# Kernel optimization log

Hardware: AMD Instinct MI355X
Metric: run time of the kernel (lower is better)

Reference implementation:

```python
import jax, jax.numpy as jnp
import numpy as np


def setup_inputs() -> dict:
    key = jax.random.key(0)
    T, B, I, H = 512, 64, 512, 512
    k = 1.0 / np.sqrt(H)
    ks = jax.random.split(key, 5)
    x = jax.random.normal(ks[0], (T, B, I), dtype=jnp.float32)
    w_ih = jax.random.uniform(ks[1], (H, I), jnp.float32, -k, k)
    w_hh = jax.random.uniform(ks[2], (H, H), jnp.float32, -k, k)
    b_ih = jax.random.uniform(ks[3], (H,), jnp.float32, -k, k)
    b_hh = jax.random.uniform(ks[4], (H,), jnp.float32, -k, k)
    return {"x": x, "w_ih": w_ih, "w_hh": w_hh, "b_ih": b_ih, "b_hh": b_hh}


def reference(x, w_ih, w_hh, b_ih, b_hh):
    # Single-layer Elman RNN, batch_first=False: x is [T, B, I].
    # h_t = tanh(x_t @ W_ih^T + b_ih + h_{t-1} @ W_hh^T + b_hh)
    T, B, _ = x.shape
    H = w_hh.shape[0]
    # Precompute input projections for all timesteps in one big GEMM.
    xproj = jnp.einsum('tbi,hi->tbh', x, w_ih) + b_ih + b_hh  # [T, B, H]

    def step(h, xp_t):
        h_new = jnp.tanh(xp_t + h @ w_hh.T)
        return h_new, h_new

    h0 = jnp.zeros((B, H), dtype=x.dtype)
    h_n, output = jax.lax.scan(step, h0, xproj)
    # torch-style h_n has a leading num_layers dim
    return output, h_n[None]
```

## Files before the change

### kernel.cpp

```cpp
#include <hip/hip_runtime.h>
#include <hip/hip_fp16.h>

#define T_STEPS 512
#define BATCH   64
#define HID     512

#define SCH_REG  40
#define SCH_LDS  10
#define SCH_SA   7
#define SCH_SB   7

#define X16_OFF   0u
#define X16_BYTES (16777216u * 2u)
#define WIH_OFF   (X16_OFF + X16_BYTES)
#define WIH_BYTES (262144u * 2u)
#define WHH_OFF   (WIH_OFF + WIH_BYTES)
#define WHH_BYTES (262144u * 2u)
#define WS_FULL   (WHH_OFF + WHH_BYTES)

typedef _Float16 half2v  __attribute__((ext_vector_type(2)));
typedef short    short8  __attribute__((ext_vector_type(8)));
typedef float    f32x4   __attribute__((ext_vector_type(4)));
union F4H { float4 f; half2v h[4]; };

__device__ inline float dot2f(half2v a, half2v b, float c) {
    return __builtin_amdgcn_fdot2(a, b, c, false);
}
__device__ inline unsigned short f2bf(float f) {
    unsigned u = __builtin_bit_cast(unsigned, f);
    return (unsigned short)((u + 0x7FFFu + ((u >> 16) & 1u)) >> 16);
}

__global__ __launch_bounds__(256) void cvt_f16(const float* __restrict__ w,
                                               __half* __restrict__ o) {
    const int i = (blockIdx.x * 256 + threadIdx.x) * 4;
    float4 v = *(const float4*)(w + i);
    __half2 p0; p0.x = __float2half(v.x); p0.y = __float2half(v.y);
    __half2 p1; p1.x = __float2half(v.z); p1.y = __float2half(v.w);
    *(__half2*)(o + i)     = p0;
    *(__half2*)(o + i + 2) = p1;
}

__global__ __launch_bounds__(256) void cvt_bf16(const float* __restrict__ s,
                                                unsigned short* __restrict__ o) {
    const int i = (blockIdx.x * 256 + threadIdx.x) * 4;
    float4 v = *(const float4*)(s + i);
    ushort4 r = {f2bf(v.x), f2bf(v.y), f2bf(v.z), f2bf(v.w)};
    *(ushort4*)(o + i) = r;
}

__global__ __launch_bounds__(256) void xproj_mfma(
    const unsigned short* __restrict__ x16,
    const unsigned short* __restrict__ w16,
    const float* __restrict__ b_ih, const float* __restrict__ b_hh,
    float* __restrict__ out)
{
    __shared__ __align__(16) unsigned short As[128][40];
    __shared__ __align__(16) unsigned short Bs[128][40];

    const int tid   = threadIdx.x;
    const int mBase = blockIdx.y * 128;
    const int nBase = blockIdx.x * 128;
    const int wave  = tid >> 6, lane = tid & 63;
    const int wy    = wave >> 1, wx = wave & 1;
    const int quad  = lane >> 4, l15 = lane & 15;
    const int lr    = tid >> 2;
    const int lk    = (tid & 3) * 8;

    f32x4 acc[4][4] = {};

    const size_t arow0 = (size_t)(mBase + lr) * 512 + lk;
    const size_t brow0 = (size_t)(nBase + lr) * 512 + lk;

    for (int k0 = 0; k0 < 512; k0 += 32) {
        int4 a0 = *(const int4*)(x16 + arow0 + k0);
        int4 a1 = *(const int4*)(x16 + arow0 + (size_t)64 * 512 + k0);
        int4 b0 = *(const int4*)(w16 + brow0 + k0);
        int4 b1 = *(const int4*)(w16 + brow0 + (size_t)64 * 512 + k0);
        __syncthreads();
        *(int4*)&As[lr][lk]      = a0;
        *(int4*)&As[lr + 64][lk] = a1;
        *(int4*)&Bs[lr][lk]      = b0;
        *(int4*)&Bs[lr + 64][lk] = b1;
        __syncthreads();

        short8 af[4], bf[4];
#pragma unroll
        for (int mt = 0; mt < 4; ++mt)
            af[mt] = *(const short8*)&As[wy * 64 + mt * 16 + l15][quad * 8];
#pragma unroll
        for (int nt = 0; nt < 4; ++nt)
            bf[nt] = *(const short8*)&Bs[wx * 64 + nt * 16 + l15][quad * 8];
#pragma unroll
        for (int mt = 0; mt < 4; ++mt)
#pragma unroll
            for (int nt = 0; nt < 4; ++nt)
                acc[mt][nt] = __builtin_amdgcn_mfma_f32_16x16x32_bf16(
                    af[mt], bf[nt], acc[mt][nt], 0, 0, 0);
    }

    float bias[4]; int coln[4];
#pragma unroll
    for (int nt = 0; nt < 4; ++nt) {
        coln[nt] = nBase + wx * 64 + nt * 16 + l15;
        bias[nt] = b_ih[coln[nt]] + b_hh[coln[nt]];
    }
#pragma unroll
    for (int mt = 0; mt < 4; ++mt)
#pragma unroll
        for (int r = 0; r < 4; ++r) {
            const int row = mBase + wy * 64 + mt * 16 + quad * 4 + r;
#pragma unroll
            for (int nt = 0; nt < 4; ++nt)
                out[(size_t)row * 512 + coln[nt]] = acc[mt][nt][r] + bias[nt];
        }
}

__global__ __launch_bounds__(256) void xproj_gemm(
    const float* __restrict__ x, const float* __restrict__ w_ih,
    const float* __restrict__ b_ih, const float* __restrict__ b_hh,
    float* __restrict__ out)
{
    __shared__ __align__(16) float As[16][68];
    __shared__ __align__(16) float Bs[16][68];

    const int tid   = threadIdx.x;
    const int tx    = tid & 15;
    const int ty    = tid >> 4;
    const int mBase = blockIdx.y * 64;
    const int nBase = blockIdx.x * 64;
    const int ldr   = tid >> 2;
    const int ldk   = (tid & 3) * 4;

    float acc[4][4] = {};
    const float* aptr = x    + (size_t)(mBase + ldr) * 512 + ldk;
    const float* bptr = w_ih + (size_t)(nBase + ldr) * 512 + ldk;

    for (int k0 = 0; k0 < 512; k0 += 16) {
        float4 av = *(const float4*)(aptr + k0);
        float4 bv = *(const float4*)(bptr + k0);
        __syncthreads();
        As[ldk + 0][ldr] = av.x; As[ldk + 1][ldr] = av.y;
        As[ldk + 2][ldr] = av.z; As[ldk + 3][ldr] = av.w;
        Bs[ldk + 0][ldr] = bv.x; Bs[ldk + 1][ldr] = bv.y;
        Bs[ldk + 2][ldr] = bv.z; Bs[ldk + 3][ldr] = bv.w;
        __syncthreads();
#pragma unroll
        for (int kk = 0; kk < 16; ++kk) {
            float4 a = *(const float4*)&As[kk][ty * 4];
            float4 b = *(const float4*)&Bs[kk][tx * 4];
            float ar[4] = {a.x, a.y, a.z, a.w};
            float br[4] = {b.x, b.y, b.z, b.w};
#pragma unroll
            for (int i = 0; i < 4; ++i)
#pragma unroll
                for (int j = 0; j < 4; ++j)
                    acc[i][j] = fmaf(ar[i], br[j], acc[i][j]);
        }
    }
    const int n0 = nBase + tx * 4;
    float bias[4];
#pragma unroll
    for (int j = 0; j < 4; ++j) bias[j] = b_ih[n0 + j] + b_hh[n0 + j];
#pragma unroll
    for (int i = 0; i < 4; ++i) {
        const int m = mBase + ty * 4 + i;
        float4 v = {acc[i][0] + bias[0], acc[i][1] + bias[1],
                    acc[i][2] + bias[2], acc[i][3] + bias[3]};
        *(float4*)(out + (size_t)m * 512 + n0) = v;
    }
}

#define ACC4(WF, G) do {                                        \
    F4H hh_; hh_.f = *(const float4*)(hrow + (G) * 8);          \
    F4H ww_; ww_.f = (WF);                                      \
    a0 = dot2f(ww_.h[0], hh_.h[0], a0);                         \
    a1 = dot2f(ww_.h[1], hh_.h[1], a1);                         \
    a2 = dot2f(ww_.h[2], hh_.h[2], a2);                         \
    a3 = dot2f(ww_.h[3], hh_.h[3], a3); } while (0)

__global__ __launch_bounds__(512)
__attribute__((amdgpu_waves_per_eu(2, 2)))
void rnn_scan4(const __half* __restrict__ w16, float* __restrict__ out)
{
    __shared__ __align__(16) float4 wlds[SCH_LDS][HID];
    __shared__ __align__(16) __half hbuf[2][HID];

    const int b = blockIdx.x;
    const int j = threadIdx.x;

    const __half* wrow = w16 + (size_t)j * HID;

    float4 wreg[SCH_REG];
#pragma unroll
    for (int c = 0; c < SCH_REG; ++c)
        wreg[c] = *(const float4*)(wrow + c * 8);

#pragma unroll
    for (int c = 0; c < SCH_LDS; ++c)
        wlds[c][j] = *(const float4*)(wrow + (SCH_REG + c) * 8);

    hbuf[0][j] = __float2half(0.f);
    __syncthreads();

    float* outb = out + (size_t)b * HID + j;
    const size_t stride = (size_t)BATCH * HID;
    const __half* wstr = wrow + (SCH_REG + SCH_LDS) * 8;

    int cur = 0;
    float hn = 0.f;
    float xp_next = outb[0];

    for (int t = 0; t < T_STEPS; ++t) {
        const float xp = xp_next;
        const int tn = (t + 1 < T_STEPS) ? (t + 1) : t;
        xp_next = outb[(size_t)tn * stride];

        const __half* hrow = hbuf[cur];

        float4 wa[SCH_SA];
#pragma unroll
        for (int c = 0; c < SCH_SA; ++c)
            wa[c] = *(const float4*)(wstr + c * 8);

        float a0 = xp, a1 = 0.f, a2 = 0.f, a3 = 0.f;

#pragma unroll
        for (int c = 0; c < 20; ++c) ACC4(wreg[c], c);

#pragma unroll
        for (int c = 0; c < SCH_SA; ++c)
            ACC4(wa[c], SCH_REG + SCH_LDS + c);

        float4 wb[SCH_SB];
#pragma unroll
        for (int c = 0; c < SCH_SB; ++c)
            wb[c] = *(const float4*)(wstr + (SCH_SA + c) * 8);

#pragma unroll
        for (int c = 20; c < SCH_REG; ++c) ACC4(wreg[c], c);
#pragma unroll
        for (int c = 0; c < SCH_LDS; ++c) {
            float4 wf = wlds[c][j];
            ACC4(wf, SCH_REG + c);
        }

#pragma unroll
        for (int c = 0; c < SCH_SB; ++c)
            ACC4(wb[c], SCH_REG + SCH_LDS + SCH_SA + c);

        float s = (a0 + a1) + (a2 + a3);
        s = fminf(fmaxf(s, -15.f), 15.f);
        const float e = __expf(2.f * s);
        hn = (e - 1.f) * __builtin_amdgcn_rcpf(e + 1.f);

        outb[(size_t)t * stride] = hn;
        hbuf[cur ^ 1][j] = __float2half(hn);
        __syncthreads();
        cur ^= 1;
    }
    out[(size_t)T_STEPS * stride + (size_t)b * HID + j] = hn;
}

__global__ __launch_bounds__(512) void rnn_scan_f32(const float* __restrict__ w,
                                                    float* __restrict__ out)
{
    __shared__ __align__(16) __half hs[2][HID];
    const int b = blockIdx.x;
    const int j = threadIdx.x;

    hs[0][j] = __float2half(0.f);
    __syncthreads();

    const float* wrow32 = w + (size_t)j * HID;
    float* outb = out + (size_t)b * HID + j;
    int cur = 0;
    float hn = 0.f;

    for (int t = 0; t < T_STEPS; ++t) {
        float a0 = outb[(size_t)t * (BATCH * HID)];
        float a1 = 0.f, a2 = 0.f, a3 = 0.f;
#pragma unroll 4
        for (int k0 = 0; k0 < HID; k0 += 8) {
            float4 w0 = *(const float4*)(wrow32 + k0);
            float4 w1 = *(const float4*)(wrow32 + k0 + 4);
            F4H h; h.f = *(const float4*)(&hs[cur][k0]);
            float2 h0 = __half22float2(*(__half2*)&h.h[0]);
            float2 h1 = __half22float2(*(__half2*)&h.h[1]);
            float2 h2 = __half22float2(*(__half2*)&h.h[2]);
            float2 h3 = __half22float2(*(__half2*)&h.h[3]);
            a0 = fmaf(w0.x, h0.x, a0); a1 = fmaf(w0.y, h0.y, a1);
            a2 = fmaf(w0.z, h1.x, a2); a3 = fmaf(w0.w, h1.y, a3);
            a0 = fmaf(w1.x, h2.x, a0); a1 = fmaf(w1.y, h2.y, a1);
            a2 = fmaf(w1.z, h3.x, a2); a3 = fmaf(w1.w, h3.y, a3);
        }
        hn = tanhf((a0 + a1) + (a2 + a3));
        outb[(size_t)t * (BATCH * HID)] = hn;
        hs[cur ^ 1][j] = __float2half(hn);
        __syncthreads();
        cur ^= 1;
    }
    out[(size_t)T_STEPS * BATCH * HID + (size_t)b * HID + j] = hn;
}

extern "C" void kernel_launch(void* const* d_in, const int* in_sizes, int n_in,
                              void* d_out, int out_size, void* d_ws, size_t ws_size,
                              hipStream_t stream) {
    const float* x    = (const float*)d_in[0];
    const float* w_ih = (const float*)d_in[1];
    const float* w_hh = (const float*)d_in[2];
    const float* b_ih = (const float*)d_in[3];
    const float* b_hh = (const float*)d_in[4];
    float* out = (float*)d_out;

    char* ws = (char*)d_ws;
    const bool full = ws_size >= (size_t)WS_FULL;
    const bool mid  = ws_size >= (size_t)WHH_BYTES;

    if (full) {
        unsigned short* x16   = (unsigned short*)(ws + X16_OFF);
        unsigned short* wih16 = (unsigned short*)(ws + WIH_OFF);
        __half*         whh16 = (__half*)(ws + WHH_OFF);
        cvt_bf16<<<16384, 256, 0, stream>>>(x, x16);
        cvt_bf16<<<256,   256, 0, stream>>>(w_ih, wih16);
        cvt_f16 <<<256,   256, 0, stream>>>(w_hh, whh16);
        xproj_mfma<<<dim3(4, 256), 256, 0, stream>>>(x16, wih16, b_ih, b_hh, out);
        rnn_scan4<<<BATCH, HID, 0, stream>>>(whh16, out);
    } else if (mid) {
        __half* whh16 = (__half*)ws;
        cvt_f16<<<256, 256, 0, stream>>>(w_hh, whh16);
        xproj_gemm<<<dim3(8, 512), 256, 0, stream>>>(x, w_ih, b_ih, b_hh, out);
        rnn_scan4<<<BATCH, HID, 0, stream>>>(whh16, out);
    } else {
        xproj_gemm<<<dim3(8, 512), 256, 0, stream>>>(x, w_ih, b_ih, b_hh, out);
        rnn_scan_f32<<<BATCH, HID, 0, stream>>>(w_hh, out);
    }
}
```

Before: 892.1 us.

## Use MFMA recurrent scan over 16-batch groups with fp16 tiled xproj

Replaces the per-batch dot2 recurrent kernel with an MFMA-based scan. Each of 4 blocks handles 16 batch rows and keeps W_hh fragments in registers and LDS, while the hidden state lives in LDS as fp16. The input conversion of x is fused into the xproj GEMM, which now writes fp16 projections in a tiled layout matched to the scan's MFMA output fragments. This removes one full pass over x and cuts the recurrent dot-product work per step. The cost is only 4 active CUs for the serial scan and extra fp16 rounding of the projections and hidden state.

```diff
diff --git a/kernel.cpp b/kernel.cpp
--- a/kernel.cpp
+++ b/kernel.cpp
@@ -4,24 +4,29 @@
 #define T_STEPS 512
 #define BATCH   64
 #define HID     512
+
+#define NB      16
+#define AK_LDS  12
 
 #define SCH_REG  40
 #define SCH_LDS  10
 #define SCH_SA   7
 #define SCH_SB   7
 
-#define X16_OFF   0u
-#define X16_BYTES (16777216u * 2u)
-#define WIH_OFF   (X16_OFF + X16_BYTES)
+#define XP16_OFF  0u
+#define XP16_BYTES (16777216u * 2u)
+#define WIH_OFF   (XP16_OFF + XP16_BYTES)
 #define WIH_BYTES (262144u * 2u)
 #define WHH_OFF   (WIH_OFF + WIH_BYTES)
 #define WHH_BYTES (262144u * 2u)
 #define WS_FULL   (WHH_OFF + WHH_BYTES)
 
 typedef _Float16 half2v  __attribute__((ext_vector_type(2)));
+typedef _Float16 half4v  __attribute__((ext_vector_type(4)));
+typedef _Float16 half8   __attribute__((ext_vector_type(8)));
 typedef short    short8  __attribute__((ext_vector_type(8)));
 typedef float    f32x4   __attribute__((ext_vector_type(4)));
-union F4H { float4 f; half2v h[4]; };
+union F4H  { float4 f; half2v h[4]; };
 
 __device__ inline float dot2f(half2v a, half2v b, float c) {
     return __builtin_amdgcn_fdot2(a, b, c, false);
@@ -50,10 +55,10 @@
 }
 
 __global__ __launch_bounds__(256) void xproj_mfma(
-    const unsigned short* __restrict__ x16,
+    const float* __restrict__ x,
     const unsigned short* __restrict__ w16,
     const float* __restrict__ b_ih, const float* __restrict__ b_hh,
-    float* __restrict__ out)
+    __half* __restrict__ xp16)
 {
     __shared__ __align__(16) unsigned short As[128][40];
     __shared__ __align__(16) unsigned short Bs[128][40];
@@ -73,13 +78,24 @@
     const size_t brow0 = (size_t)(nBase + lr) * 512 + lk;
 
     for (int k0 = 0; k0 < 512; k0 += 32) {
-        int4 a0 = *(const int4*)(x16 + arow0 + k0);
-        int4 a1 = *(const int4*)(x16 + arow0 + (size_t)64 * 512 + k0);
+        float4 a0l = *(const float4*)(x + arow0 + k0);
+        float4 a0h = *(const float4*)(x + arow0 + k0 + 4);
+        float4 a1l = *(const float4*)(x + arow0 + (size_t)64 * 512 + k0);
+        float4 a1h = *(const float4*)(x + arow0 + (size_t)64 * 512 + k0 + 4);
         int4 b0 = *(const int4*)(w16 + brow0 + k0);
         int4 b1 = *(const int4*)(w16 + brow0 + (size_t)64 * 512 + k0);
-        __syncthreads();
-        *(int4*)&As[lr][lk]      = a0;
-        *(int4*)&As[lr + 64][lk] = a1;
+        int4 A0, A1;
+        A0.x = f2bf(a0l.x) | ((unsigned)f2bf(a0l.y) << 16);
+        A0.y = f2bf(a0l.z) | ((unsigned)f2bf(a0l.w) << 16);
+        A0.z = f2bf(a0h.x) | ((unsigned)f2bf(a0h.y) << 16);
+        A0.w = f2bf(a0h.z) | ((unsigned)f2bf(a0h.w) << 16);
+        A1.x = f2bf(a1l.x) | ((unsigned)f2bf(a1l.y) << 16);
+        A1.y = f2bf(a1l.z) | ((unsigned)f2bf(a1l.w) << 16);
+        A1.z = f2bf(a1h.x) | ((unsigned)f2bf(a1h.y) << 16);
+        A1.w = f2bf(a1h.z) | ((unsigned)f2bf(a1h.w) << 16);
+        __syncthreads();
+        *(int4*)&As[lr][lk]      = A0;
+        *(int4*)&As[lr + 64][lk] = A1;
         *(int4*)&Bs[lr][lk]      = b0;
         *(int4*)&Bs[lr + 64][lk] = b1;
         __syncthreads();
@@ -109,10 +125,15 @@
     for (int mt = 0; mt < 4; ++mt)
 #pragma unroll
         for (int r = 0; r < 4; ++r) {
-            const int row = mBase + wy * 64 + mt * 16 + quad * 4 + r;
-#pragma unroll
-            for (int nt = 0; nt < 4; ++nt)
-                out[(size_t)row * 512 + coln[nt]] = acc[mt][nt][r] + bias[nt];
+            const int m = mBase + wy * 64 + mt * 16 + quad * 4 + r;
+            const int tt = m >> 6, b = m & 63;
+#pragma unroll
+            for (int nt = 0; nt < 4; ++nt) {
+                const int o = coln[nt];
+                const size_t idx = (size_t)tt * 32768 + (size_t)(b >> 4) * 8192
+                                 + (o >> 3) * 128 + (b & 15) * 8 + (o & 7);
+                xp16[idx] = __float2half(acc[mt][nt][r] + bias[nt]);
+            }
         }
 }
 
@@ -171,6 +192,138 @@
     }
 }
 
+#define PIN8(a) asm volatile("" : "+v"(a[0]), "+v"(a[1]), "+v"(a[2]), "+v"(a[3]), \
+                                  "+v"(a[4]), "+v"(a[5]), "+v"(a[6]), "+v"(a[7]))
+
+__global__ __launch_bounds__(512)
+__attribute__((amdgpu_waves_per_eu(2, 2)))
+void rnn_scan6(const __half* __restrict__ whh16,
+               const __half* __restrict__ xp16,
+               float* __restrict__ out)
+{
+    __shared__ __align__(16) _Float16 hlds[64 * NB * 8];
+    __shared__ __align__(16) _Float16 alds[8 * AK_LDS * 512];
+
+    const int bg   = blockIdx.x;
+    const int tid  = threadIdx.x;
+    const int w    = tid >> 6;
+    const int lane = tid & 63;
+    const int q    = lane >> 4;
+    const int l15  = lane & 15;
+
+    const __half* wbase = whh16 + ((size_t)(64 * w + l15)) * 512 + 8 * q;
+    half8 wf0[16], wf1[16], wf2[16], wf3[4];
+#pragma unroll
+    for (int ki = 0; ki < 16; ++ki) {
+        wf0[ki] = *(const half8*)(wbase + 32 * ki);
+        wf1[ki] = *(const half8*)(wbase + (size_t)16 * 512 + 32 * ki);
+        wf2[ki] = *(const half8*)(wbase + (size_t)32 * 512 + 32 * ki);
+    }
+#pragma unroll
+    for (int ki = 0; ki < 4; ++ki)
+        wf3[ki] = *(const half8*)(wbase + (size_t)48 * 512 + 32 * (12 + ki));
+#pragma unroll
+    for (int ki = 0; ki < AK_LDS; ++ki) {
+        half8 v = *(const half8*)(wbase + (size_t)48 * 512 + 32 * ki);
+        *(half8*)&alds[(w * AK_LDS + ki) * 512 + lane * 8] = v;
+    }
+    {
+        float4 z = {0.f, 0.f, 0.f, 0.f};
+        *(float4*)&hlds[tid * 16]     = z;
+        *(float4*)&hlds[tid * 16 + 8] = z;
+    }
+    __syncthreads();
+
+    int cidx[4];
+#pragma unroll
+    for (int ta = 0; ta < 4; ++ta)
+        cidx[ta] = (8 * w + 2 * ta + (q >> 1)) * 128 + l15 * 8 + (q & 1) * 4;
+
+    const __half* xpb = xp16 + (size_t)bg * 8192;
+
+    const int sb  = tid >> 5, so = (tid & 31) * 16;
+    const int hrd = ((tid & 31) * 2) * 128 + sb * 8;
+    float* outb = out + (size_t)(bg * 16 + sb) * 512 + so;
+    const size_t ostride = (size_t)BATCH * HID;
+
+    for (int t = 0; t < T_STEPS; ++t) {
+        uint2 xpv0 = *(const uint2*)(xpb + (size_t)t * 32768 + cidx[0]);
+        uint2 xpv1 = *(const uint2*)(xpb + (size_t)t * 32768 + cidx[1]);
+        uint2 xpv2 = *(const uint2*)(xpb + (size_t)t * 32768 + cidx[2]);
+        uint2 xpv3 = *(const uint2*)(xpb + (size_t)t * 32768 + cidx[3]);
+
+        if (t > 0) {
+            half8 h0 = *(const half8*)&hlds[hrd];
+            half8 h1 = *(const half8*)&hlds[hrd + 128];
+            float* dst = outb + (size_t)(t - 1) * ostride;
+            float4 v0 = {(float)h0[0], (float)h0[1], (float)h0[2], (float)h0[3]};
+            float4 v1 = {(float)h0[4], (float)h0[5], (float)h0[6], (float)h0[7]};
+            float4 v2 = {(float)h1[0], (float)h1[1], (float)h1[2], (float)h1[3]};
+            float4 v3 = {(float)h1[4], (float)h1[5], (float)h1[6], (float)h1[7]};
+            *(float4*)(dst)      = v0;
+            *(float4*)(dst + 4)  = v1;
+            *(float4*)(dst + 8)  = v2;
+            *(float4*)(dst + 12) = v3;
+        }
+
+        f32x4 acc0 = {0.f, 0.f, 0.f, 0.f};
+        f32x4 acc1 = {0.f, 0.f, 0.f, 0.f};
+        f32x4 acc2 = {0.f, 0.f, 0.f, 0.f};
+        f32x4 acc3 = {0.f, 0.f, 0.f, 0.f};
+#pragma unroll
+        for (int ki = 0; ki < 16; ++ki) {
+            half8 bfr = *(const half8*)&hlds[(4 * ki + q) * 128 + l15 * 8];
+            acc0 = __builtin_amdgcn_mfma_f32_16x16x32_f16(wf0[ki], bfr, acc0, 0, 0, 0);
+            acc1 = __builtin_amdgcn_mfma_f32_16x16x32_f16(wf1[ki], bfr, acc1, 0, 0, 0);
+            acc2 = __builtin_amdgcn_mfma_f32_16x16x32_f16(wf2[ki], bfr, acc2, 0, 0, 0);
+            half8 a3;
+            if (ki < AK_LDS)
+                a3 = *(const half8*)&alds[(w * AK_LDS + ki) * 512 + lane * 8];
+            else
+                a3 = wf3[ki - AK_LDS];
+            acc3 = __builtin_amdgcn_mfma_f32_16x16x32_f16(a3, bfr, acc3, 0, 0, 0);
+        }
+        __syncthreads();
+
+#pragma unroll
+        for (int ta = 0; ta < 4; ++ta) {
+            const uint2 xv = (ta == 0) ? xpv0 : (ta == 1) ? xpv1
+                           : (ta == 2) ? xpv2 : xpv3;
+            const half4v xh = __builtin_bit_cast(half4v, xv);
+            const f32x4 A = (ta == 0) ? acc0 : (ta == 1) ? acc1
+                          : (ta == 2) ? acc2 : acc3;
+            half4v hv;
+#pragma unroll
+            for (int r = 0; r < 4; ++r) {
+                float s = A[r] + (float)xh[r];
+                s = fminf(fmaxf(s, -15.f), 15.f);
+                const float e = __expf(2.f * s);
+                hv[r] = (_Float16)((e - 1.f) * __builtin_amdgcn_rcpf(e + 1.f));
+            }
+            *(half4v*)&hlds[cidx[ta]] = hv;
+        }
+        PIN8(wf0); PIN8((wf0 + 8)); PIN8(wf1); PIN8((wf1 + 8));
+        PIN8(wf2); PIN8((wf2 + 8));
+        asm volatile("" : "+v"(wf3[0]), "+v"(wf3[1]), "+v"(wf3[2]), "+v"(wf3[3]));
+        __syncthreads();
+    }
+
+    {
+        half8 h0 = *(const half8*)&hlds[hrd];
+        half8 h1 = *(const half8*)&hlds[hrd + 128];
+        float4 v0 = {(float)h0[0], (float)h0[1], (float)h0[2], (float)h0[3]};
+        float4 v1 = {(float)h0[4], (float)h0[5], (float)h0[6], (float)h0[7]};
+        float4 v2 = {(float)h1[0], (float)h1[1], (float)h1[2], (float)h1[3]};
+        float4 v3 = {(float)h1[4], (float)h1[5], (float)h1[6], (float)h1[7]};
+        float* d0 = outb + (size_t)(T_STEPS - 1) * ostride;
+        float* d1 = outb + (size_t)T_STEPS * ostride;
+        *(float4*)(d0)      = v0; *(float4*)(d0 + 4)  = v1;
+        *(float4*)(d0 + 8)  = v2; *(float4*)(d0 + 12) = v3;
+        *(float4*)(d1)      = v0; *(float4*)(d1 + 4)  = v1;
+        *(float4*)(d1 + 8)  = v2; *(float4*)(d1 + 12) = v3;
+    }
+}
+
 #define ACC4(WF, G) do {                                        \
     F4H hh_; hh_.f = *(const float4*)(hrow + (G) * 8);          \
     F4H ww_; ww_.f = (WF);                                      \
@@ -227,7 +380,6 @@
 
 #pragma unroll
         for (int c = 0; c < 20; ++c) ACC4(wreg[c], c);
-
 #pragma unroll
         for (int c = 0; c < SCH_SA; ++c)
             ACC4(wa[c], SCH_REG + SCH_LDS + c);
@@ -241,8 +393,8 @@
         for (int c = 20; c < SCH_REG; ++c) ACC4(wreg[c], c);
 #pragma unroll
         for (int c = 0; c < SCH_LDS; ++c) {
-            float4 wf = wlds[c][j];
-            ACC4(wf, SCH_REG + c);
+            float4 wfv = wlds[c][j];
+            ACC4(wfv, SCH_REG + c);
         }
 
 #pragma unroll
@@ -318,14 +470,13 @@
     const bool mid  = ws_size >= (size_t)WHH_BYTES;
 
     if (full) {
-        unsigned short* x16   = (unsigned short*)(ws + X16_OFF);
+        __half*         xp16  = (__half*)(ws + XP16_OFF);
         unsigned short* wih16 = (unsigned short*)(ws + WIH_OFF);
         __half*         whh16 = (__half*)(ws + WHH_OFF);
-        cvt_bf16<<<16384, 256, 0, stream>>>(x, x16);
-        cvt_bf16<<<256,   256, 0, stream>>>(w_ih, wih16);
-        cvt_f16 <<<256,   256, 0, stream>>>(w_hh, whh16);
-        xproj_mfma<<<dim3(4, 256), 256, 0, stream>>>(x16, wih16, b_ih, b_hh, out);
-        rnn_scan4<<<BATCH, HID, 0, stream>>>(whh16, out);
+        cvt_bf16<<<256, 256, 0, stream>>>(w_ih, wih16);
+        cvt_f16 <<<256, 256, 0, stream>>>(w_hh, whh16);
+        xproj_mfma<<<dim3(4, 256), 256, 0, stream>>>(x, wih16, b_ih, b_hh, xp16);
+        rnn_scan6<<<4, 512, 0, stream>>>(whh16, xp16, out);
     } else if (mid) {
         __half* whh16 = (__half*)ws;
         cvt_f16<<<256, 256, 0, stream>>>(w_hh, whh16);
```

Measured after the change: 1.420 ms. 1.59x slower.
